# Performance work log

Measured on AMD Instinct MI355X. Metric: run time of the kernel, lower is better.

## Reference

```python
import jax, jax.numpy as jnp
import numpy as np

H = W = 512
A = 256  # number of projection angles


def setup_inputs() -> dict:
    key = jax.random.key(0)
    k1, k2 = jax.random.split(key)
    data = jax.random.normal(k1, (1, 1, H, W), dtype=jnp.float32)
    # angles uniform in [0, pi) -- realistic tomographic scan range
    angles = jax.random.uniform(k2, (A,), dtype=jnp.float32) * np.float32(np.pi)
    return {"data": data, "angles": angles}


def _radon(data, angles):
    B, C, h, w = data.shape  # B == C == 1 structurally required by the torch module
    nA = angles.shape[0]
    cos = jnp.cos(angles)
    sin = jnp.sin(angles)

    # F.affine_grid(align_corners=False) base coordinates: pixel centers in [-1, 1]
    xs = (2.0 * jnp.arange(w, dtype=data.dtype) + 1.0) / w - 1.0  # [W]
    ys = (2.0 * jnp.arange(h, dtype=data.dtype) + 1.0) / h - 1.0  # [H]
    by, bx = jnp.meshgrid(ys, xs, indexing="ij")  # [H,W]

    # theta built from -angles: rows [cos a, sin a, 0; -sin a, cos a, 0]
    gx = cos[:, None, None] * bx + sin[:, None, None] * by  # [A,H,W]
    gy = -sin[:, None, None] * bx + cos[:, None, None] * by  # [A,H,W]

    # grid_sample(align_corners=False): unnormalize to input pixel coords
    ix = ((gx + 1.0) * w - 1.0) * 0.5
    iy = ((gy + 1.0) * h - 1.0) * 0.5

    x0 = jnp.floor(ix).astype(jnp.int32)
    y0 = jnp.floor(iy).astype(jnp.int32)
    x1 = x0 + 1
    y1 = y0 + 1
    wx1 = ix - x0.astype(data.dtype)
    wx0 = 1.0 - wx1
    wy1 = iy - y0.astype(data.dtype)
    wy0 = 1.0 - wy1

    img = data[0, 0]  # [H,W]

    def gather(yy, xx):
        # zero padding: out-of-range taps contribute 0
        valid = (xx >= 0) & (xx < w) & (yy >= 0) & (yy < h)
        v = img[jnp.clip(yy, 0, h - 1), jnp.clip(xx, 0, w - 1)]
        return jnp.where(valid, v, jnp.zeros((), data.dtype))

    rotated = (wy0 * (wx0 * gather(y0, x0) + wx1 * gather(y0, x1))
               + wy1 * (wx0 * gather(y1, x0) + wx1 * gather(y1, x1)))  # [A,H,W]

    proj = jnp.sum(rotated, axis=1)  # sum over height -> [A,W]
    return proj.reshape(1, 1, nA, w)


def reference(data, angles):
    return _radon(data, angles)
```

## Files before the change

### kernel.cpp

```cpp
#include <hip/hip_runtime.h>


#define HH 512
#define WW 512
#define NA 256
#define XC 64
#define YC 64
#define NXC (WW / XC)
#define NYC (HH / YC)
#define NW 8
#define ROWS_MAX 92
#define STRIDE_MAX 97
#define PAD 112
#define PW (WW + 2 * PAD)
#define PH (HH + 2 * PAD)

__global__ __launch_bounds__(256) void pad_kernel(
    const float* __restrict__ img, float* __restrict__ P)
{
    const int c = blockIdx.x * 256 + threadIdx.x;
    const int r = blockIdx.y;
    if (c >= PW) return;
    const int gr = r - PAD, gc = c - PAD;
    float v = 0.0f;
    if ((unsigned)gr < (unsigned)HH && (unsigned)gc < (unsigned)WW)
        v = img[gr * WW + gc];
    P[r * PW + c] = v;
}

template <bool PADDED>
__global__ __launch_bounds__(512, 8) void radon_kernel(
    const float* __restrict__ src,
    const float* __restrict__ angles, float* __restrict__ out)
{
    __shared__ float tile[ROWS_MAX * STRIDE_MAX];

    const int tid  = threadIdx.x;
    const int lane = tid & 63;
    const int wid  = tid >> 6;

    const int a  = blockIdx.x >> 3;
    const int x0 = (blockIdx.x & 7) * XC;

    float s, c;
    sincosf(angles[a], &s, &c);

    const int stride = (c >= 0.0f) ? 95 : 97;

    const float u  = (float)(x0 + lane) + (0.5f - 256.0f);
    const float u0 = (float)x0 + (0.5f - 256.0f);
    const float u1 = u0 + (float)(XC - 1);

    const float* __restrict__ Porg = src + PAD * PW + PAD;

    float acc = 0.0f;

    for (int yc = 0; yc < NYC; ++yc) {
        const float v0 = (float)(yc * YC) + (0.5f - 256.0f);
        const float v1 = v0 + (float)(YC - 1);

        const float cu0 = c * u0, cu1 = c * u1;
        const float sv0 = s * v0, sv1 = s * v1;
        const float su0 = -s * u0, su1 = -s * u1;
        const float cv0 = c * v0, cv1 = c * v1;

        const float cx_min = fminf(cu0, cu1) + fminf(sv0, sv1) + 255.5f;
        const float cx_max = fmaxf(cu0, cu1) + fmaxf(sv0, sv1) + 255.5f;
        const float rx_min = fminf(su0, su1) + fminf(cv0, cv1) + 255.5f;
        const float rx_max = fmaxf(su0, su1) + fmaxf(cv0, cv1) + 255.5f;

        const int c_lo = (int)floorf(cx_min);
        const int c_hi = (int)floorf(cx_max) + 1;
        const int r_lo = (int)floorf(rx_min);
        const int r_hi = (int)floorf(rx_max) + 1;
        int bh = min(r_hi - r_lo + 1, ROWS_MAX);

        if (c_lo > WW - 1 || c_hi < 0 || r_lo > HH - 1 || r_hi < 0) continue;

        __syncthreads();

        if (PADDED) {
            if (lane < 23) {
                for (int r = wid; r < bh; r += NW) {
                    const float* g = Porg + (r_lo + r) * PW + c_lo + lane * 4;
                    float* l = &tile[r * stride];
                    __builtin_amdgcn_global_load_lds(
                        (__attribute__((address_space(1))) const void*)g,
                        (__attribute__((address_space(3))) void*)l, 16, 0, 0);
                }
            }
        } else {
            const int bw = min(c_hi - c_lo + 1, STRIDE_MAX);
            for (int r = wid; r < bh; r += NW) {
                const int gr = r_lo + r;
                const bool row_ok = ((unsigned)gr < (unsigned)HH);
                const float* __restrict__ rowp = src + gr * WW;
                for (int cc = lane; cc < bw; cc += 64) {
                    const int gc = c_lo + cc;
                    float v = 0.0f;
                    if (row_ok) {
                        const int gcl = min(max(gc, 0), WW - 1);
                        const float t = rowp[gcl];
                        v = ((unsigned)gc < (unsigned)WW) ? t : 0.0f;
                    }
                    tile[r * stride + cc] = v;
                }
            }
        }

        __syncthreads();

        const float bc = fmaf(c, u, 255.5f - (float)c_lo);
        const float br = fmaf(-s, u, 255.5f - (float)r_lo);
        float vy = v0 + (float)(wid * 8);

#pragma unroll
        for (int i = 0; i < 8; ++i) {
            const float cxl = fmaf(s, vy, bc);
            const float rxl = fmaf(c, vy, br);
            const int ci = (int)cxl;
            const int ri = (int)rxl;
#if __has_builtin(__builtin_amdgcn_fractf)
            const float wx1 = __builtin_amdgcn_fractf(cxl);
            const float wy1 = __builtin_amdgcn_fractf(rxl);
#else
            const float wx1 = cxl - floorf(cxl);
            const float wy1 = rxl - floorf(rxl);
#endif
            const float wx0 = 1.0f - wx1;
            const float wy0 = 1.0f - wy1;

            __builtin_assume(ri >= 0 && ri < ROWS_MAX);
            __builtin_assume(ci >= 0 && ci < STRIDE_MAX);
            const int ad = ri * stride + ci;

            const float v00 = tile[ad];
            const float v01 = tile[ad + 1];
            const float v10 = tile[ad + stride];
            const float v11 = tile[ad + stride + 1];

            acc = fmaf(wy0, fmaf(wx1, v01, wx0 * v00), acc);
            acc = fmaf(wy1, fmaf(wx1, v11, wx0 * v10), acc);
            vy += 1.0f;
        }
    }

    __syncthreads();
    tile[tid] = acc;
    __syncthreads();
    if (tid < 64) {
        float r = tile[tid];
#pragma unroll
        for (int k = 1; k < NW; ++k) r += tile[k * 64 + tid];
        out[a * WW + x0 + tid] = r;
    }
}

extern "C" void kernel_launch(void* const* d_in, const int* in_sizes, int n_in,
                              void* d_out, int out_size, void* d_ws, size_t ws_size,
                              hipStream_t stream) {
    const float* img    = (const float*)d_in[0];
    const float* angles = (const float*)d_in[1];
    float* out = (float*)d_out;
    float* P   = (float*)d_ws;

    const bool padded = (ws_size >= (size_t)PW * PH * sizeof(float));

    if (padded) {
        pad_kernel<<<dim3((PW + 255) / 256, PH), 256, 0, stream>>>(img, P);
        radon_kernel<true><<<dim3(NA * NXC), 512, 0, stream>>>(P, angles, out);
    } else {
        radon_kernel<false><<<dim3(NA * NXC), 512, 0, stream>>>(img, angles, out);
    }
}
```

Measured before the change: 110.4 us.

## Template LDS stride, fixed-count unrolled tile loads, and packed-FMA bilinear accumulation

Result: no change. 111.4 us (+0.9%).

```diff
diff --git a/kernel.cpp b/kernel.cpp
--- a/kernel.cpp
+++ b/kernel.cpp
@@ -6,14 +6,16 @@
 #define NA 256
 #define XC 64
 #define YC 64
-#define NXC (WW / XC)
-#define NYC (HH / YC)
+#define NXC 8
+#define NYC 8
 #define NW 8
-#define ROWS_MAX 92
-#define STRIDE_MAX 97
+#define RM 96
+#define SM 97
 #define PAD 112
 #define PW (WW + 2 * PAD)
 #define PH (HH + 2 * PAD)
+
+typedef float f32x2 __attribute__((ext_vector_type(2)));
 
 __global__ __launch_bounds__(256) void pad_kernel(
     const float* __restrict__ img, float* __restrict__ P)
@@ -28,12 +30,120 @@
     P[r * PW + c] = v;
 }
 
+template <int S, bool PADDED>
+__device__ __forceinline__ float radon_chunks(
+    const float* __restrict__ src, float* __restrict__ tile,
+    const float s, const float c, const int lane, const int wid, const int x0)
+{
+    const float u  = (float)(x0 + lane) + (0.5f - 256.0f);
+    const float u0 = (float)x0 + (0.5f - 256.0f);
+    const float u1 = u0 + 63.0f;
+
+    const float cu0 = c * u0, cu1 = c * u1;
+    const float cumin = fminf(cu0, cu1), cumax = fmaxf(cu0, cu1);
+    const float su0 = -s * u0, su1 = -s * u1;
+    const float sumin = fminf(su0, su1), sumax = fmaxf(su0, su1);
+
+    const float bcc = fmaf(c, u, 255.5f);
+    const float brc = fmaf(-s, u, 255.5f);
+
+    const float* __restrict__ Porg =
+        PADDED ? (src + PAD * PW + PAD) : src;
+
+    f32x2 accT = {0.0f, 0.0f}, accB = {0.0f, 0.0f};
+
+    for (int yc = 0; yc < NYC; ++yc) {
+        const float v0 = (float)(yc * YC) + (0.5f - 256.0f);
+        const float v1 = v0 + 63.0f;
+
+        const float sv0 = s * v0, sv1 = s * v1;
+        const float cv0 = c * v0, cv1 = c * v1;
+        const float cvmin = fminf(cv0, cv1), cvmax = fmaxf(cv0, cv1);
+
+        const float cx_min = cumin + sv0 + 255.5f;
+        const float cx_max = cumax + sv1 + 255.5f;
+        const float rx_min = sumin + cvmin + 255.5f;
+        const float rx_max = sumax + cvmax + 255.5f;
+
+        const int c_lo = (int)floorf(cx_min);
+        const int c_hi = (int)floorf(cx_max) + 1;
+        const int r_lo = (int)floorf(rx_min);
+        const int r_hi = (int)floorf(rx_max) + 1;
+
+        if (c_lo > WW - 1 || c_hi < 0 || r_lo > HH - 1 || r_hi < 0) continue;
+
+        __syncthreads();
+
+        if (PADDED) {
+            if (lane < 23) {
+                const float* g = Porg + (r_lo + wid) * PW + c_lo + lane * 4;
+                int loff = wid * S;
+#pragma unroll
+                for (int k = 0; k < 12; ++k) {
+                    __builtin_amdgcn_global_load_lds(
+                        (const __attribute__((address_space(1))) void*)g,
+                        (__attribute__((address_space(3))) void*)&tile[loff],
+                        16, 0, 0);
+                    g += NW * PW;
+                    loff += NW * S;
+                }
+            }
+        } else {
+            for (int r = wid; r < RM; r += NW) {
+                const int gr = r_lo + r;
+                const bool row_ok = ((unsigned)gr < (unsigned)HH);
+                const float* __restrict__ rowp = src + gr * WW;
+                for (int cc = lane; cc < 92; cc += 64) {
+                    const int gc = c_lo + cc;
+                    float v = 0.0f;
+                    if (row_ok && (unsigned)gc < (unsigned)WW)
+                        v = rowp[gc];
+                    tile[r * S + cc] = v;
+                }
+            }
+        }
+
+        __syncthreads();
+
+        const float bc = bcc - (float)c_lo;
+        const float br = brc - (float)r_lo;
+        const float vyb = v0 + (float)(wid * 8);
+        const float cx0 = fmaf(s, vyb, bc);
+        const float rx0 = fmaf(c, vyb, br);
+
+#pragma unroll
+        for (int i = 0; i < 8; ++i) {
+            const float cxl = fmaf(s, (float)i, cx0);
+            const float rxl = fmaf(c, (float)i, rx0);
+            const int ci = (int)cxl;
+            const int ri = (int)rxl;
+            const float wx1 = __builtin_amdgcn_fractf(cxl);
+            const float wy1 = __builtin_amdgcn_fractf(rxl);
+            const float wy0 = 1.0f - wy1;
+
+            __builtin_assume(ri >= 0 && ri < RM - 1);
+            __builtin_assume(ci >= 0 && ci < 92);
+            const int ad = ri * S + ci;
+
+            f32x2 vt, vb;
+            vt.x = tile[ad];     vt.y = tile[ad + 1];
+            vb.x = tile[ad + S]; vb.y = tile[ad + S + 1];
+
+            const f32x2 wx = {1.0f - wx1, wx1};
+            accT = __builtin_elementwise_fma(wx * wy0, vt, accT);
+            accB = __builtin_elementwise_fma(wx * wy1, vb, accB);
+        }
+    }
+
+    return (accT.x + accT.y) + (accB.x + accB.y);
+}
+
 template <bool PADDED>
 __global__ __launch_bounds__(512, 8) void radon_kernel(
     const float* __restrict__ src,
     const float* __restrict__ angles, float* __restrict__ out)
 {
-    __shared__ float tile[ROWS_MAX * STRIDE_MAX];
+    __shared__ float tile[RM * SM];
 
     const int tid  = threadIdx.x;
     const int lane = tid & 63;
@@ -45,105 +155,11 @@
     float s, c;
     sincosf(angles[a], &s, &c);
 
-    const int stride = (c >= 0.0f) ? 95 : 97;
-
-    const float u  = (float)(x0 + lane) + (0.5f - 256.0f);
-    const float u0 = (float)x0 + (0.5f - 256.0f);
-    const float u1 = u0 + (float)(XC - 1);
-
-    const float* __restrict__ Porg = src + PAD * PW + PAD;
-
-    float acc = 0.0f;
-
-    for (int yc = 0; yc < NYC; ++yc) {
-        const float v0 = (float)(yc * YC) + (0.5f - 256.0f);
-        const float v1 = v0 + (float)(YC - 1);
-
-        const float cu0 = c * u0, cu1 = c * u1;
-        const float sv0 = s * v0, sv1 = s * v1;
-        const float su0 = -s * u0, su1 = -s * u1;
-        const float cv0 = c * v0, cv1 = c * v1;
-
-        const float cx_min = fminf(cu0, cu1) + fminf(sv0, sv1) + 255.5f;
-        const float cx_max = fmaxf(cu0, cu1) + fmaxf(sv0, sv1) + 255.5f;
-        const float rx_min = fminf(su0, su1) + fminf(cv0, cv1) + 255.5f;
-        const float rx_max = fmaxf(su0, su1) + fmaxf(cv0, cv1) + 255.5f;
-
-        const int c_lo = (int)floorf(cx_min);
-        const int c_hi = (int)floorf(cx_max) + 1;
-        const int r_lo = (int)floorf(rx_min);
-        const int r_hi = (int)floorf(rx_max) + 1;
-        int bh = min(r_hi - r_lo + 1, ROWS_MAX);
-
-        if (c_lo > WW - 1 || c_hi < 0 || r_lo > HH - 1 || r_hi < 0) continue;
-
-        __syncthreads();
-
-        if (PADDED) {
-            if (lane < 23) {
-                for (int r = wid; r < bh; r += NW) {
-                    const float* g = Porg + (r_lo + r) * PW + c_lo + lane * 4;
-                    float* l = &tile[r * stride];
-                    __builtin_amdgcn_global_load_lds(
-                        (__attribute__((address_space(1))) const void*)g,
-                        (__attribute__((address_space(3))) void*)l, 16, 0, 0);
-                }
-            }
-        } else {
-            const int bw = min(c_hi - c_lo + 1, STRIDE_MAX);
-            for (int r = wid; r < bh; r += NW) {
-                const int gr = r_lo + r;
-                const bool row_ok = ((unsigned)gr < (unsigned)HH);
-                const float* __restrict__ rowp = src + gr * WW;
-                for (int cc = lane; cc < bw; cc += 64) {
-                    const int gc = c_lo + cc;
-                    float v = 0.0f;
-                    if (row_ok) {
-                        const int gcl = min(max(gc, 0), WW - 1);
-                        const float t = rowp[gcl];
-                        v = ((unsigned)gc < (unsigned)WW) ? t : 0.0f;
-                    }
-                    tile[r * stride + cc] = v;
-                }
-            }
-        }
-
-        __syncthreads();
-
-        const float bc = fmaf(c, u, 255.5f - (float)c_lo);
-        const float br = fmaf(-s, u, 255.5f - (float)r_lo);
-        float vy = v0 + (float)(wid * 8);
-
-#pragma unroll
-        for (int i = 0; i < 8; ++i) {
-            const float cxl = fmaf(s, vy, bc);
-            const float rxl = fmaf(c, vy, br);
-            const int ci = (int)cxl;
-            const int ri = (int)rxl;
-#if __has_builtin(__builtin_amdgcn_fractf)
-            const float wx1 = __builtin_amdgcn_fractf(cxl);
-            const float wy1 = __builtin_amdgcn_fractf(rxl);
-#else
-            const float wx1 = cxl - floorf(cxl);
-            const float wy1 = rxl - floorf(rxl);
-#endif
-            const float wx0 = 1.0f - wx1;
-            const float wy0 = 1.0f - wy1;
-
-            __builtin_assume(ri >= 0 && ri < ROWS_MAX);
-            __builtin_assume(ci >= 0 && ci < STRIDE_MAX);
-            const int ad = ri * stride + ci;
-
-            const float v00 = tile[ad];
-            const float v01 = tile[ad + 1];
-            const float v10 = tile[ad + stride];
-            const float v11 = tile[ad + stride + 1];
-
-            acc = fmaf(wy0, fmaf(wx1, v01, wx0 * v00), acc);
-            acc = fmaf(wy1, fmaf(wx1, v11, wx0 * v10), acc);
-            vy += 1.0f;
-        }
-    }
+    float acc;
+    if (c >= 0.0f)
+        acc = radon_chunks<95, PADDED>(src, tile, s, c, lane, wid, x0);
+    else
+        acc = radon_chunks<97, PADDED>(src, tile, s, c, lane, wid, x0);
 
     __syncthreads();
     tile[tid] = acc;
```
